# Optimization experiments

Hardware: AMD Instinct MI355X
Metric: run time of the kernel (lower is better)

## Reference

```python
import jax, jax.numpy as jnp
import numpy as np
import math

B, S, D, H = 2, 2048, 2048, 16
HD = D // H            # 128
FF = 4 * D             # 8192
EPS = 1e-5


def _alibi_slopes(num_heads):
    # power-of-2 path (16 heads): slopes = base^i, base = 2^(-2^-(log2(n)-3))
    closest = 2 ** math.floor(math.log2(num_heads))
    base = 2.0 ** (-(2.0 ** (-(math.log2(closest) - 3))))
    powers = np.arange(1, 1 + closest, dtype=np.float32)
    slopes = base ** powers
    if closest != num_heads:
        extra_base = 2.0 ** (-(2.0 ** (-(math.log2(2 * closest) - 3))))
        num_rem = min(closest, num_heads - closest)
        extra_powers = np.arange(1, 1 + 2 * num_rem, 2, dtype=np.float32)
        slopes = np.concatenate([slopes, extra_base ** extra_powers])
    return jnp.asarray(slopes, dtype=jnp.float32)


def setup_inputs() -> dict:
    key = jax.random.key(0)
    ks = jax.random.split(key, 8)
    s = 0.02
    return {
        "x": jax.random.normal(ks[0], (B, S, D), dtype=jnp.float32),
        "ln1_w": jnp.ones((D,), jnp.float32),
        "ln1_b": jnp.zeros((D,), jnp.float32),
        "wqkv": jax.random.normal(ks[1], (D, 3 * D), jnp.float32) * s,
        "bqkv": jnp.zeros((3 * D,), jnp.float32),
        "wo": jax.random.normal(ks[2], (D, D), jnp.float32) * s,
        "bo": jnp.zeros((D,), jnp.float32),
        "ln2_w": jnp.ones((D,), jnp.float32),
        "ln2_b": jnp.zeros((D,), jnp.float32),
        "w1": jax.random.normal(ks[3], (D, FF), jnp.float32) * s,
        "b1": jnp.zeros((FF,), jnp.float32),
        "w2": jax.random.normal(ks[4], (FF, D), jnp.float32) * s,
        "b2": jnp.zeros((D,), jnp.float32),
    }


def _ln(x, w, b):
    mu = jnp.mean(x, axis=-1, keepdims=True)
    var = jnp.mean(jnp.square(x - mu), axis=-1, keepdims=True)
    return (x - mu) * jax.lax.rsqrt(var + EPS) * w + b


def reference(x, ln1_w, ln1_b, wqkv, bqkv, wo, bo, ln2_w, ln2_b, w1, b1, w2, b2):
    slopes = _alibi_slopes(H)                      # [H]
    # --- input layernorm + attention ---
    h = _ln(x, ln1_w, ln1_b)
    qkv = h @ wqkv + bqkv                          # [B,S,3D]
    q, k, v = jnp.split(qkv, 3, axis=-1)
    q = q.reshape(B, S, H, HD).transpose(0, 2, 1, 3)  # [B,H,S,HD]
    k = k.reshape(B, S, H, HD).transpose(0, 2, 1, 3)
    v = v.reshape(B, S, H, HD).transpose(0, 2, 1, 3)
    scores = jnp.einsum("bhqd,bhkd->bhqk", q, k) / math.sqrt(HD)
    pos = jnp.arange(S, dtype=jnp.float32)
    rel = pos[None, :] - pos[:, None]              # j - i
    alibi = slopes[:, None, None] * rel[None]      # [H,S,S]
    scores = scores.astype(jnp.float32) + alibi[None]
    causal = rel <= 0                              # j <= i
    scores = jnp.where(causal[None, None], scores, jnp.finfo(jnp.float32).min)
    probs = jax.nn.softmax(scores, axis=-1).astype(x.dtype)
    attn = jnp.einsum("bhqk,bhkd->bhqd", probs, v)  # [B,H,S,HD]
    attn = attn.transpose(0, 2, 1, 3).reshape(B, S, D)
    x = x + attn @ wo + bo
    # --- post-attn layernorm + GELU MLP ---
    h2 = _ln(x, ln2_w, ln2_b)
    m = jax.nn.gelu(h2 @ w1 + b1, approximate=True) @ w2 + b2
    return x + m
```

## Files before the change

### kernel.cpp

```cpp
#include <hip/hip_runtime.h>
#include <hip/hip_bf16.h>
#include <stdint.h>

#define BB 2
#define SS 2048
#define DD 2048
#define HH 16
#define HD 128
#define FFD 8192
#define TD (3*DD)

typedef unsigned short u16;
typedef __attribute__((ext_vector_type(8))) short s16x8;
typedef __attribute__((ext_vector_type(4))) float f32x4;

struct alignas(8) U16x4 { u16 a, b, c, d; };

__device__ __forceinline__ u16 f2b(float f) {
  union { float f; uint32_t u; } v; v.f = f;
  uint32_t r = (v.u + 0x7fffu + ((v.u >> 16) & 1u)) >> 16;
  return (u16)r;
}

__device__ __forceinline__ void async16(const void* g, void* l) {
  __builtin_amdgcn_global_load_lds((const __attribute__((address_space(1))) void*)g,
                                   (__attribute__((address_space(3))) void*)l,
                                   16, 0, 0);
}

__global__ __launch_bounds__(256) void wconv_t(const float* __restrict__ W,
                                               u16* __restrict__ Wt, int K, int N) {
  __shared__ float tile[64][65];
  int k0 = blockIdx.x * 64, n0 = blockIdx.y * 64;
  int c = threadIdx.x & 63, r0 = threadIdx.x >> 6;
#pragma unroll
  for (int i = 0; i < 16; ++i) {
    int r = i * 4 + r0;
    tile[r][c] = W[(size_t)(k0 + r) * N + n0 + c];
  }
  __syncthreads();
#pragma unroll
  for (int i = 0; i < 16; ++i) {
    int n = i * 4 + r0;
    Wt[(size_t)(n0 + n) * K + k0 + c] = f2b(tile[c][n]);
  }
}

__global__ __launch_bounds__(256) void ln_kernel(const float* __restrict__ X,
                                                 const float* __restrict__ g,
                                                 const float* __restrict__ be,
                                                 u16* __restrict__ O) {
  int row = blockIdx.x;
  const float* xr = X + (size_t)row * DD;
  int t = threadIdx.x;
  float4 v0 = ((const float4*)xr)[t];
  float4 v1 = ((const float4*)xr)[t + 256];
  float s = v0.x + v0.y + v0.z + v0.w + v1.x + v1.y + v1.z + v1.w;
  float q = v0.x*v0.x + v0.y*v0.y + v0.z*v0.z + v0.w*v0.w
          + v1.x*v1.x + v1.y*v1.y + v1.z*v1.z + v1.w*v1.w;
#pragma unroll
  for (int o = 32; o > 0; o >>= 1) { s += __shfl_down(s, o); q += __shfl_down(q, o); }
  __shared__ float red[8];
  if ((t & 63) == 0) { red[t >> 6] = s; red[4 + (t >> 6)] = q; }
  __syncthreads();
  float S = red[0] + red[1] + red[2] + red[3];
  float Q = red[4] + red[5] + red[6] + red[7];
  float mu = S * (1.0f / DD);
  float var = Q * (1.0f / DD) - mu * mu;
  float rs = rsqrtf(var + 1e-5f);
  float4 g0 = ((const float4*)g)[t],  g1 = ((const float4*)g)[t + 256];
  float4 b0 = ((const float4*)be)[t], b1 = ((const float4*)be)[t + 256];
  U16x4 o0, o1;
  o0.a = f2b((v0.x - mu) * rs * g0.x + b0.x);
  o0.b = f2b((v0.y - mu) * rs * g0.y + b0.y);
  o0.c = f2b((v0.z - mu) * rs * g0.z + b0.z);
  o0.d = f2b((v0.w - mu) * rs * g0.w + b0.w);
  o1.a = f2b((v1.x - mu) * rs * g1.x + b1.x);
  o1.b = f2b((v1.y - mu) * rs * g1.y + b1.y);
  o1.c = f2b((v1.z - mu) * rs * g1.z + b1.z);
  o1.d = f2b((v1.w - mu) * rs * g1.w + b1.w);
  *(U16x4*)(O + (size_t)row * DD + t * 4)         = o0;
  *(U16x4*)(O + (size_t)row * DD + (t + 256) * 4) = o1;
}

template <int MODE>
__global__ __launch_bounds__(512, 2) void gemm8(const u16* __restrict__ A,
                                                const u16* __restrict__ Bt,
                                                const float* __restrict__ bias,
                                                const float* __restrict__ res,
                                                void* __restrict__ Cout,
                                                int M, int N, int K) {
  __shared__ __align__(16) u16 As[2][2][256 * 32];
  __shared__ __align__(16) u16 Bs[2][2][128 * 32];

  int n0 = blockIdx.x * 128, m0 = blockIdx.y * 256;
  int tid = threadIdx.x;
  int lane = tid & 63, w = tid >> 6;
  int wn = w & 1, wm = w >> 1;
  int col = lane & 15, quad = lane >> 4;

  int r = tid >> 2, sl = tid & 3;
  int gks = (sl ^ ((r >> 1) & 3)) * 8;
  const u16* ag = A  + (size_t)(m0 + r) * K + gks;
  const u16* bg = Bt + (size_t)(n0 + r) * K + gks;

  int swz = (col >> 1) & 3;
  int aoff = (wm * 64) * 32 + col * 32 + ((quad ^ swz) * 8);
  int boff = (wn * 64) * 32 + col * 32 + ((quad ^ swz) * 8);

  f32x4 acc[4][4] = {};
  int ntiles = K >> 6;

#pragma unroll
  for (int kh = 0; kh < 2; ++kh) {
    async16(ag + kh * 32, &As[0][kh][tid * 8]);
    async16(ag + (size_t)128 * K + kh * 32, &As[0][kh][4096 + tid * 8]);
    async16(bg + kh * 32, &Bs[0][kh][tid * 8]);
  }
  asm volatile("s_waitcnt vmcnt(0)" ::: "memory");
  __builtin_amdgcn_s_barrier();

  for (int t = 0; t < ntiles; ++t) {
    int p = t & 1, pn = p ^ 1;
    const u16* agn = ag + (t + 1) * 64;
    const u16* bgn = bg + (t + 1) * 64;
    bool pf = (t + 1 < ntiles);
#pragma unroll
    for (int kh = 0; kh < 2; ++kh) {
      const u16* as_ = As[p][kh];
      const u16* bs_ = Bs[p][kh];
      s16x8 af[4], bf[4];
#pragma unroll
      for (int i = 0; i < 4; ++i)
        bf[i] = *(const s16x8*)&bs_[boff + i * 512];
#pragma unroll
      for (int i = 0; i < 4; ++i)
        af[i] = *(const s16x8*)&as_[aoff + i * 512];
      if (pf) {
        async16(agn + kh * 32, &As[pn][kh][tid * 8]);
        async16(agn + (size_t)128 * K + kh * 32, &As[pn][kh][4096 + tid * 8]);
        async16(bgn + kh * 32, &Bs[pn][kh][tid * 8]);
        asm volatile("s_waitcnt vmcnt(3)" ::: "memory");
      } else if (kh == 0) {
        asm volatile("s_waitcnt vmcnt(0)" ::: "memory");
      }
      __builtin_amdgcn_s_barrier();
      __builtin_amdgcn_s_setprio(1);
#pragma unroll
      for (int i = 0; i < 4; ++i)
#pragma unroll
        for (int j = 0; j < 4; ++j)
          acc[i][j] = __builtin_amdgcn_mfma_f32_16x16x32_bf16(
              af[i], bf[j], acc[i][j], 0, 0, 0);
      __builtin_amdgcn_s_setprio(0);
      __builtin_amdgcn_s_barrier();
    }
  }

#pragma unroll
  for (int mt = 0; mt < 4; ++mt) {
    int mg = m0 + wm * 64 + mt * 16 + quad * 4;
#pragma unroll
    for (int nt = 0; nt < 4; ++nt) {
      int ng = n0 + wn * 64 + nt * 16 + col;
      float bn = bias[ng];
#pragma unroll
      for (int rr = 0; rr < 4; ++rr) {
        float v = acc[mt][nt][rr] + bn;
        size_t idx = (size_t)(mg + rr) * N + ng;
        if (MODE == 1) {
          float u = 1.5957691216057308f * (v + 0.044715f * v * v * v);
          v = v / (1.0f + __expf(-u));
        }
        if (MODE == 2) {
          ((float*)Cout)[idx] = v + res[idx];
        } else {
          ((u16*)Cout)[idx] = f2b(v);
        }
      }
    }
  }
}

template <int MODE>
__global__ __launch_bounds__(512, 2) void gemm256(const u16* __restrict__ A,
                                                  const u16* __restrict__ Bt,
                                                  const float* __restrict__ bias,
                                                  const float* __restrict__ res,
                                                  void* __restrict__ Cout,
                                                  int M, int N, int K) {
  __shared__ __align__(16) u16 As[2][2][256 * 32];
  __shared__ __align__(16) u16 Bs[2][2][256 * 32];

  int n0 = blockIdx.x * 256, m0 = blockIdx.y * 256;
  int tid = threadIdx.x;
  int lane = tid & 63, w = tid >> 6;
  int wn = w & 3, wm = w >> 2;
  int col = lane & 15, quad = lane >> 4;

  int r = tid >> 2, sl = tid & 3;
  int gks = (sl ^ ((r >> 1) & 3)) * 8;
  const u16* ag = A  + (size_t)(m0 + r) * K + gks;
  const u16* bg = Bt + (size_t)(n0 + r) * K + gks;

  int swz = (col >> 1) & 3;
  int aoff = (wm * 128 + col) * 32 + ((quad ^ swz) * 8);
  int boff = (wn * 64 + col) * 32 + ((quad ^ swz) * 8);

  f32x4 acc[8][4] = {};
  int ntiles = K >> 6;

#pragma unroll
  for (int kh = 0; kh < 2; ++kh) {
    async16(ag + kh * 32, &As[0][kh][tid * 8]);
    async16(ag + (size_t)128 * K + kh * 32, &As[0][kh][4096 + tid * 8]);
    async16(bg + kh * 32, &Bs[0][kh][tid * 8]);
    async16(bg + (size_t)128 * K + kh * 32, &Bs[0][kh][4096 + tid * 8]);
  }
  asm volatile("s_waitcnt vmcnt(0)" ::: "memory");
  __builtin_amdgcn_s_barrier();

  for (int t = 0; t < ntiles; ++t) {
    int p = t & 1, pn = p ^ 1;
    const u16* agn = ag + (t + 1) * 64;
    const u16* bgn = bg + (t + 1) * 64;
    bool pf = (t + 1 < ntiles);
#pragma unroll
    for (int kh = 0; kh < 2; ++kh) {
      const u16* as_ = As[p][kh];
      const u16* bs_ = Bs[p][kh];
      s16x8 bf[4];
#pragma unroll
      for (int j = 0; j < 4; ++j)
        bf[j] = *(const s16x8*)&bs_[boff + j * 512];
#pragma unroll
      for (int q = 0; q < 2; ++q) {
        s16x8 af[4];
#pragma unroll
        for (int i = 0; i < 4; ++i)
          af[i] = *(const s16x8*)&as_[aoff + q * 2048 + i * 512];
        if (pf) {
          if (q == 0) {
            async16(agn + kh * 32, &As[pn][kh][tid * 8]);
            async16(agn + (size_t)128 * K + kh * 32, &As[pn][kh][4096 + tid * 8]);
          } else {
            async16(bgn + kh * 32, &Bs[pn][kh][tid * 8]);
            async16(bgn + (size_t)128 * K + kh * 32, &Bs[pn][kh][4096 + tid * 8]);
            asm volatile("s_waitcnt vmcnt(4)" ::: "memory");
          }
        } else if (kh == 0 && q == 1) {
          asm volatile("s_waitcnt vmcnt(0)" ::: "memory");
        }
        __builtin_amdgcn_s_barrier();
        __builtin_amdgcn_s_setprio(1);
#pragma unroll
        for (int i = 0; i < 4; ++i)
#pragma unroll
          for (int j = 0; j < 4; ++j)
            acc[q * 4 + i][j] = __builtin_amdgcn_mfma_f32_16x16x32_bf16(
                af[i], bf[j], acc[q * 4 + i][j], 0, 0, 0);
        __builtin_amdgcn_s_setprio(0);
        __builtin_amdgcn_s_barrier();
      }
    }
  }

#pragma unroll
  for (int mt = 0; mt < 8; ++mt) {
    int mg = m0 + wm * 128 + mt * 16 + quad * 4;
#pragma unroll
    for (int nt = 0; nt < 4; ++nt) {
      int ng = n0 + wn * 64 + nt * 16 + col;
      float bn = bias[ng];
#pragma unroll
      for (int rr = 0; rr < 4; ++rr) {
        float v = acc[mt][nt][rr] + bn;
        size_t idx = (size_t)(mg + rr) * N + ng;
        if (MODE == 1) {
          float u = 1.5957691216057308f * (v + 0.044715f * v * v * v);
          v = v / (1.0f + __expf(-u));
        }
        if (MODE == 2) {
          ((float*)Cout)[idx] = v + res[idx];
        } else {
          ((u16*)Cout)[idx] = f2b(v);
        }
      }
    }
  }
}

__global__ __launch_bounds__(256) void attn_kernel(const u16* __restrict__ qkv,
                                                   u16* __restrict__ out) {
  __shared__ __align__(16) u16 Ks[2][64 * 128];
  __shared__ __align__(16) u16 Vts[128 * 64];
  __shared__ __align__(16) u16 Ps[4][16 * 72];
  int bx = blockIdx.x, h = blockIdx.y, b = blockIdx.z;
  int tid = threadIdx.x, lane = tid & 63, w = tid >> 6;
  int col = lane & 15, quad = lane >> 4;
  const u16* base  = qkv + (size_t)b * SS * TD + (size_t)h * HD;
  const u16* kbase = base + DD;
  const u16* vbase = base + 2 * DD;
  float slope = exp2f(-0.5f * (float)(h + 1));
  const float scale = 0.088388347648318447f;
  int krow = tid >> 4;
  int ghb = (tid & 15) ^ (krow & 7);
  int vkey_loc = tid >> 4;
  int vhd0 = (tid & 15) * 8;
  int kxc = 8 * (tid & 7);

#pragma unroll 1
  for (int ph = 0; ph < 2; ++ph) {
    int qt = ph ? (31 - bx) : bx;
    int q0 = qt * 64;
    int ntile = qt + 1;
    int qr = q0 + w * 16 + col;
    s16x8 qf[4];
#pragma unroll
    for (int c = 0; c < 4; ++c)
      qf[c] = *(const s16x8*)(base + (size_t)qr * TD + c * 32 + quad * 8);
    float m_i[4] = {-1e30f, -1e30f, -1e30f, -1e30f};
    float l_i[4] = {0.f, 0.f, 0.f, 0.f};
    f32x4 oacc[8] = {};
#pragma unroll
    for (int s = 0; s < 4; ++s)
      async16(kbase + (size_t)(s * 16 + krow) * TD + ghb * 8,
              &Ks[0][s * 2048 + tid * 8]);
    s16x8 vreg[4];
#pragma unroll
    for (int s = 0; s < 4; ++s)
      vreg[s] = *(const s16x8*)(vbase + (size_t)(s * 16 + vkey_loc) * TD + vhd0);

    for (int t = 0; t < ntile; ++t) {
      int j0 = t * 64;
      __syncthreads();
      if (t + 1 < ntile) {
#pragma unroll
        for (int s = 0; s < 4; ++s)
          async16(kbase + (size_t)(j0 + 64 + s * 16 + krow) * TD + ghb * 8,
                  &Ks[(t + 1) & 1][s * 2048 + tid * 8]);
      }
#pragma unroll
      for (int s = 0; s < 4; ++s) {
        int key = s * 16 + vkey_loc;
#pragma unroll
        for (int j = 0; j < 8; ++j)
          Vts[(vhd0 + j) * 64 + (key ^ kxc)] = (u16)vreg[s][j];
      }
      if (t + 1 < ntile) {
#pragma unroll
        for (int s = 0; s < 4; ++s)
          vreg[s] = *(const s16x8*)(vbase + (size_t)(j0 + 64 + s * 16 + vkey_loc) * TD + vhd0);
      }
      const u16* kt_ = Ks[t & 1];
      f32x4 sc[4];
#pragma unroll
      for (int nt = 0; nt < 4; ++nt) {
        f32x4 s4 = {0.f, 0.f, 0.f, 0.f};
        int key = nt * 16 + col;
        int ksw = col & 7;
#pragma unroll
        for (int c = 0; c < 4; ++c) {
          s16x8 kf = *(const s16x8*)&kt_[key * 128 + (((c * 4 + quad) ^ ksw) * 8)];
          s4 = __builtin_amdgcn_mfma_f32_16x16x32_bf16(qf[c], kf, s4, 0, 0, 0);
        }
        sc[nt] = s4;
      }
      int rb = q0 + w * 16 + quad * 4;
      float p[4][4];
      float mt_[4] = {-1e30f, -1e30f, -1e30f, -1e30f};
#pragma unroll
      for (int nt = 0; nt < 4; ++nt) {
        int j = j0 + nt * 16 + col;
#pragma unroll
        for (int rr = 0; rr < 4; ++rr) {
          float v = sc[nt][rr] * scale + slope * (float)(j - (rb + rr));
          if (j > rb + rr) v = -1e30f;
          p[nt][rr] = v;
          mt_[rr] = fmaxf(mt_[rr], v);
        }
      }
#pragma unroll
      for (int o = 1; o < 16; o <<= 1)
#pragma unroll
        for (int rr = 0; rr < 4; ++rr) mt_[rr] = fmaxf(mt_[rr], __shfl_xor(mt_[rr], o));
      float alpha[4];
#pragma unroll
      for (int rr = 0; rr < 4; ++rr) {
        float mn = fmaxf(m_i[rr], mt_[rr]);
        alpha[rr] = __expf(m_i[rr] - mn);
        m_i[rr] = mn;
      }
      float ls[4] = {0.f, 0.f, 0.f, 0.f};
#pragma unroll
      for (int nt = 0; nt < 4; ++nt)
#pragma unroll
        for (int rr = 0; rr < 4; ++rr) {
          float e = __expf(p[nt][rr] - m_i[rr]);
          p[nt][rr] = e;
          ls[rr] += e;
        }
#pragma unroll
      for (int o = 1; o < 16; o <<= 1)
#pragma unroll
        for (int rr = 0; rr < 4; ++rr) ls[rr] += __shfl_xor(ls[rr], o);
#pragma unroll
      for (int rr = 0; rr < 4; ++rr) l_i[rr] = l_i[rr] * alpha[rr] + ls[rr];
#pragma unroll
      for (int ot = 0; ot < 8; ++ot)
#pragma unroll
        for (int rr = 0; rr < 4; ++rr) oacc[ot][rr] *= alpha[rr];
#pragma unroll
      for (int nt = 0; nt < 4; ++nt)
#pragma unroll
        for (int rr = 0; rr < 4; ++rr)
          Ps[w][(quad * 4 + rr) * 72 + nt * 16 + col] = f2b(p[nt][rr]);
      __syncthreads();
#pragma unroll
      for (int kt = 0; kt < 2; ++kt) {
        s16x8 pf = *(const s16x8*)&Ps[w][col * 72 + kt * 32 + quad * 8];
        int k8 = kt * 32 + quad * 8;
#pragma unroll
        for (int ot = 0; ot < 8; ++ot) {
          int hd = ot * 16 + col;
          int swz = 8 * ((hd >> 3) & 7);
          s16x8 vf = *(const s16x8*)&Vts[hd * 64 + (k8 ^ swz)];
          oacc[ot] = __builtin_amdgcn_mfma_f32_16x16x32_bf16(pf, vf, oacc[ot], 0, 0, 0);
        }
      }
    }
#pragma unroll
    for (int rr = 0; rr < 4; ++rr) l_i[rr] = 1.0f / l_i[rr];
    u16* ob = out + ((size_t)b * SS + q0 + w * 16 + quad * 4) * DD + h * HD;
#pragma unroll
    for (int ot = 0; ot < 8; ++ot)
#pragma unroll
      for (int rr = 0; rr < 4; ++rr)
        ob[(size_t)rr * DD + ot * 16 + col] = f2b(oacc[ot][rr] * l_i[rr]);
  }
}

extern "C" void kernel_launch(void* const* d_in, const int* in_sizes, int n_in,
                              void* d_out, int out_size, void* d_ws, size_t ws_size,
                              hipStream_t stream) {
  const float* x    = (const float*)d_in[0];
  const float* ln1w = (const float*)d_in[1];
  const float* ln1b = (const float*)d_in[2];
  const float* wqkv = (const float*)d_in[3];
  const float* bqkv = (const float*)d_in[4];
  const float* wo   = (const float*)d_in[5];
  const float* bo   = (const float*)d_in[6];
  const float* ln2w = (const float*)d_in[7];
  const float* ln2b = (const float*)d_in[8];
  const float* w1   = (const float*)d_in[9];
  const float* b1   = (const float*)d_in[10];
  const float* w2   = (const float*)d_in[11];
  const float* b2   = (const float*)d_in[12];

  const int M = BB * SS;
  char* ws = (char*)d_ws;
  u16*  wt   = (u16*)ws;
  u16*  qkv  = (u16*)(ws + 33554432ull);
  u16*  cbuf = (u16*)(ws + 33554432ull + 50331648ull);
  float* r1  = (float*)(ws + 33554432ull + 50331648ull + 67108864ull);
  u16* h1 = cbuf;
  u16* attn = cbuf;
  u16* m1 = cbuf;
  u16* h2 = qkv;

  ln_kernel<<<M, 256, 0, stream>>>(x, ln1w, ln1b, h1);
  wconv_t<<<dim3(DD / 64, TD / 64), 256, 0, stream>>>(wqkv, wt, DD, TD);
  gemm256<0><<<dim3(TD / 256, M / 256), 512, 0, stream>>>(h1, wt, bqkv, nullptr, qkv, M, TD, DD);
  attn_kernel<<<dim3(16, HH, BB), 256, 0, stream>>>(qkv, attn);
  wconv_t<<<dim3(DD / 64, DD / 64), 256, 0, stream>>>(wo, wt, DD, DD);
  gemm8<2><<<dim3(DD / 128, M / 256), 512, 0, stream>>>(attn, wt, bo, x, r1, M, DD, DD);
  ln_kernel<<<M, 256, 0, stream>>>(r1, ln2w, ln2b, h2);
  wconv_t<<<dim3(DD / 64, FFD / 64), 256, 0, stream>>>(w1, wt, DD, FFD);
  gemm256<1><<<dim3(FFD / 256, M / 256), 512, 0, stream>>>(h2, wt, b1, nullptr, m1, M, FFD, DD);
  wconv_t<<<dim3(FFD / 64, DD / 64), 256, 0, stream>>>(w2, wt, FFD, DD);
  gemm8<2><<<dim3(DD / 128, M / 256), 512, 0, stream>>>(m1, wt, b2, r1, (float*)d_out, M, DD, FFD);
}
```

Before: 854.6 us.

## Split-K the FFN down-projection with 256-tile GEMM and reduce kernel

The final MLP down-projection (K=8192) now runs on the 256x256 gemm256 kernel with a two-way split-K over blockIdx.z. Each half writes fp32 partials, one to a scratch buffer and one to the output, and a new reduce2 kernel adds them together with bias and residual. The main loop of gemm256 is also manually unrolled by two K-tiles so the double-buffer indices are compile-time constants. This is meant to give the down-projection enough blocks (8x16x2) to fill the GPU and to use the more efficient large tile. The cost is extra fp32 partial traffic and one more launch.

```diff
diff --git a/kernel.cpp b/kernel.cpp
--- a/kernel.cpp
+++ b/kernel.cpp
@@ -186,13 +186,15 @@
 __global__ __launch_bounds__(512, 2) void gemm256(const u16* __restrict__ A,
                                                   const u16* __restrict__ Bt,
                                                   const float* __restrict__ bias,
-                                                  const float* __restrict__ res,
-                                                  void* __restrict__ Cout,
-                                                  int M, int N, int K) {
+                                                  void* __restrict__ C0,
+                                                  void* __restrict__ C1,
+                                                  int M, int N, int K, int Kloc) {
   __shared__ __align__(16) u16 As[2][2][256 * 32];
   __shared__ __align__(16) u16 Bs[2][2][256 * 32];
 
   int n0 = blockIdx.x * 256, m0 = blockIdx.y * 256;
+  int kseg = blockIdx.z;
+  void* Cout = kseg ? C1 : C0;
   int tid = threadIdx.x;
   int lane = tid & 63, w = tid >> 6;
   int wn = w & 3, wm = w >> 2;
@@ -200,15 +202,15 @@
 
   int r = tid >> 2, sl = tid & 3;
   int gks = (sl ^ ((r >> 1) & 3)) * 8;
-  const u16* ag = A  + (size_t)(m0 + r) * K + gks;
-  const u16* bg = Bt + (size_t)(n0 + r) * K + gks;
+  const u16* ag = A  + (size_t)(m0 + r) * K + (size_t)kseg * Kloc + gks;
+  const u16* bg = Bt + (size_t)(n0 + r) * K + (size_t)kseg * Kloc + gks;
 
   int swz = (col >> 1) & 3;
   int aoff = (wm * 128 + col) * 32 + ((quad ^ swz) * 8);
   int boff = (wn * 64 + col) * 32 + ((quad ^ swz) * 8);
 
   f32x4 acc[8][4] = {};
-  int ntiles = K >> 6;
+  int ntiles = Kloc >> 6;
 
 #pragma unroll
   for (int kh = 0; kh < 2; ++kh) {
@@ -220,50 +222,74 @@
   asm volatile("s_waitcnt vmcnt(0)" ::: "memory");
   __builtin_amdgcn_s_barrier();
 
-  for (int t = 0; t < ntiles; ++t) {
-    int p = t & 1, pn = p ^ 1;
-    const u16* agn = ag + (t + 1) * 64;
-    const u16* bgn = bg + (t + 1) * 64;
-    bool pf = (t + 1 < ntiles);
-#pragma unroll
-    for (int kh = 0; kh < 2; ++kh) {
-      const u16* as_ = As[p][kh];
-      const u16* bs_ = Bs[p][kh];
-      s16x8 bf[4];
-#pragma unroll
-      for (int j = 0; j < 4; ++j)
-        bf[j] = *(const s16x8*)&bs_[boff + j * 512];
-#pragma unroll
-      for (int q = 0; q < 2; ++q) {
-        s16x8 af[4];
-#pragma unroll
-        for (int i = 0; i < 4; ++i)
-          af[i] = *(const s16x8*)&as_[aoff + q * 2048 + i * 512];
-        if (pf) {
-          if (q == 0) {
-            async16(agn + kh * 32, &As[pn][kh][tid * 8]);
-            async16(agn + (size_t)128 * K + kh * 32, &As[pn][kh][4096 + tid * 8]);
-          } else {
-            async16(bgn + kh * 32, &Bs[pn][kh][tid * 8]);
-            async16(bgn + (size_t)128 * K + kh * 32, &Bs[pn][kh][4096 + tid * 8]);
-            asm volatile("s_waitcnt vmcnt(4)" ::: "memory");
-          }
-        } else if (kh == 0 && q == 1) {
-          asm volatile("s_waitcnt vmcnt(0)" ::: "memory");
-        }
-        __builtin_amdgcn_s_barrier();
-        __builtin_amdgcn_s_setprio(1);
-#pragma unroll
-        for (int i = 0; i < 4; ++i)
-#pragma unroll
-          for (int j = 0; j < 4; ++j)
-            acc[q * 4 + i][j] = __builtin_amdgcn_mfma_f32_16x16x32_bf16(
-                af[i], bf[j], acc[q * 4 + i][j], 0, 0, 0);
-        __builtin_amdgcn_s_setprio(0);
-        __builtin_amdgcn_s_barrier();
-      }
-    }
-  }
+  const u16* agn = ag + 64;
+  const u16* bgn = bg + 64;
+
+#define KT256(P, PN, PF)                                                     \
+  {                                                                          \
+    const bool pf_ = (PF);                                                   \
+    _Pragma("unroll")                                                        \
+    for (int kh = 0; kh < 2; ++kh) {                                         \
+      const u16* as_ = As[P][kh];                                            \
+      const u16* bs_ = Bs[P][kh];                                            \
+      s16x8 bf[4];                                                           \
+      _Pragma("unroll")                                                      \
+      for (int j = 0; j < 4; ++j)                                            \
+        bf[j] = *(const s16x8*)&bs_[boff + j * 512];                         \
+      {                                                                      \
+        s16x8 af[4];                                                         \
+        _Pragma("unroll")                                                    \
+        for (int i = 0; i < 4; ++i)                                          \
+          af[i] = *(const s16x8*)&as_[aoff + i * 512];                       \
+        if (pf_) {                                                           \
+          async16(agn + kh * 32, &As[PN][kh][tid * 8]);                      \
+          async16(agn + (size_t)128 * K + kh * 32, &As[PN][kh][4096 + tid * 8]); \
+        }                                                                    \
+        __builtin_amdgcn_s_barrier();                                        \
+        __builtin_amdgcn_s_setprio(1);                                       \
+        _Pragma("unroll")                                                    \
+        for (int i = 0; i < 4; ++i)                                          \
+          _Pragma("unroll")                                                  \
+          for (int j = 0; j < 4; ++j)                                        \
+            acc[i][j] = __builtin_amdgcn_mfma_f32_16x16x32_bf16(             \
+                af[i], bf[j], acc[i][j], 0, 0, 0);                           \
+        __builtin_amdgcn_s_setprio(0);                                       \
+        __builtin_amdgcn_s_barrier();                                        \
+      }                                                                      \
+      {                                                                      \
+        s16x8 af[4];                                                         \
+        _Pragma("unroll")                                                    \
+        for (int i = 0; i < 4; ++i)                                          \
+          af[i] = *(const s16x8*)&as_[aoff + 2048 + i * 512];                \
+        if (pf_) {                                                           \
+          async16(bgn + kh * 32, &Bs[PN][kh][tid * 8]);                      \
+          async16(bgn + (size_t)128 * K + kh * 32, &Bs[PN][kh][4096 + tid * 8]); \
+          asm volatile("s_waitcnt vmcnt(4)" ::: "memory");                   \
+        } else if (kh == 0) {                                                \
+          asm volatile("s_waitcnt vmcnt(0)" ::: "memory");                   \
+        }                                                                    \
+        __builtin_amdgcn_s_barrier();                                        \
+        __builtin_amdgcn_s_setprio(1);                                       \
+        _Pragma("unroll")                                                    \
+        for (int i = 0; i < 4; ++i)                                          \
+          _Pragma("unroll")                                                  \
+          for (int j = 0; j < 4; ++j)                                        \
+            acc[4 + i][j] = __builtin_amdgcn_mfma_f32_16x16x32_bf16(         \
+                af[i], bf[j], acc[4 + i][j], 0, 0, 0);                       \
+        __builtin_amdgcn_s_setprio(0);                                       \
+        __builtin_amdgcn_s_barrier();                                        \
+      }                                                                      \
+    }                                                                        \
+  }
+
+  for (int t = 0; t < ntiles; t += 2) {
+    bool pf1 = (t + 2 < ntiles);
+    KT256(0, 1, true);
+    agn += 64; bgn += 64;
+    KT256(1, 0, pf1);
+    agn += 64; bgn += 64;
+  }
+#undef KT256
 
 #pragma unroll
   for (int mt = 0; mt < 8; ++mt) {
@@ -271,7 +297,7 @@
 #pragma unroll
     for (int nt = 0; nt < 4; ++nt) {
       int ng = n0 + wn * 64 + nt * 16 + col;
-      float bn = bias[ng];
+      float bn = (MODE == 3) ? 0.0f : bias[ng];
 #pragma unroll
       for (int rr = 0; rr < 4; ++rr) {
         float v = acc[mt][nt][rr] + bn;
@@ -280,14 +306,33 @@
           float u = 1.5957691216057308f * (v + 0.044715f * v * v * v);
           v = v / (1.0f + __expf(-u));
         }
-        if (MODE == 2) {
-          ((float*)Cout)[idx] = v + res[idx];
+        if (MODE == 3) {
+          ((float*)Cout)[idx] = v;
         } else {
           ((u16*)Cout)[idx] = f2b(v);
         }
       }
     }
   }
+}
+
+__global__ __launch_bounds__(256) void reduce2(const float* __restrict__ P0,
+                                               const float* P1,
+                                               const float* __restrict__ bias,
+                                               const float* __restrict__ res,
+                                               float* out, int N) {
+  size_t i = (size_t)blockIdx.x * 256 + threadIdx.x;
+  float4 a = ((const float4*)P0)[i];
+  float4 b = ((const float4*)P1)[i];
+  float4 rr = ((const float4*)res)[i];
+  int col = (int)((i * 4) % (size_t)N);
+  float4 bb = *(const float4*)&bias[col];
+  float4 o;
+  o.x = a.x + b.x + rr.x + bb.x;
+  o.y = a.y + b.y + rr.y + bb.y;
+  o.z = a.z + b.z + rr.z + bb.z;
+  o.w = a.w + b.w + rr.w + bb.w;
+  ((float4*)out)[i] = o;
 }
 
 __global__ __launch_bounds__(256) void attn_kernel(const u16* __restrict__ qkv,
@@ -467,16 +512,18 @@
   u16* attn = cbuf;
   u16* m1 = cbuf;
   u16* h2 = qkv;
+  float* p0 = (float*)qkv;
 
   ln_kernel<<<M, 256, 0, stream>>>(x, ln1w, ln1b, h1);
   wconv_t<<<dim3(DD / 64, TD / 64), 256, 0, stream>>>(wqkv, wt, DD, TD);
-  gemm256<0><<<dim3(TD / 256, M / 256), 512, 0, stream>>>(h1, wt, bqkv, nullptr, qkv, M, TD, DD);
+  gemm256<0><<<dim3(TD / 256, M / 256), 512, 0, stream>>>(h1, wt, bqkv, qkv, nullptr, M, TD, DD, DD);
   attn_kernel<<<dim3(16, HH, BB), 256, 0, stream>>>(qkv, attn);
   wconv_t<<<dim3(DD / 64, DD / 64), 256, 0, stream>>>(wo, wt, DD, DD);
   gemm8<2><<<dim3(DD / 128, M / 256), 512, 0, stream>>>(attn, wt, bo, x, r1, M, DD, DD);
   ln_kernel<<<M, 256, 0, stream>>>(r1, ln2w, ln2b, h2);
   wconv_t<<<dim3(DD / 64, FFD / 64), 256, 0, stream>>>(w1, wt, DD, FFD);
-  gemm256<1><<<dim3(FFD / 256, M / 256), 512, 0, stream>>>(h2, wt, b1, nullptr, m1, M, FFD, DD);
+  gemm256<1><<<dim3(FFD / 256, M / 256), 512, 0, stream>>>(h2, wt, b1, m1, nullptr, M, FFD, DD, DD);
   wconv_t<<<dim3(FFD / 64, DD / 64), 256, 0, stream>>>(w2, wt, FFD, DD);
-  gemm8<2><<<dim3(DD / 128, M / 256), 512, 0, stream>>>(m1, wt, b2, r1, (float*)d_out, M, DD, FFD);
-}
+  gemm256<3><<<dim3(DD / 256, M / 256, 2), 512, 0, stream>>>(m1, wt, nullptr, p0, d_out, M, DD, FFD, FFD / 2);
+  reduce2<<<(M * DD / 4) / 256, 256, 0, stream>>>(p0, (const float*)d_out, b2, r1, (float*)d_out, DD);
+}
```

New measurement: 875.2 us. +2.4%, slower.
